# Optimization experiments

Hardware: AMD Instinct MI355X
Metric: run time of the kernel (lower is better)

The kernel has to match this reference:

```python
import jax, jax.numpy as jnp
import numpy as np

WS = 7          # window size (fixed: last_idx=169=(2*7-1)^2)
NP = 1          # num_priorset
NH = 8          # num heads
DIM = 256
SHIFT = 3
N = WS * WS     # 49 tokens per window
NK = N + 3 * NP # 52 K/V tokens (window + uk/fg/bg priors)


def _rel_index():
    coords = np.stack(np.meshgrid(np.arange(WS), np.arange(WS), indexing='ij')).reshape(2, -1)
    rel = (coords[:, :, None] - coords[:, None, :]).transpose(1, 2, 0).astype(np.int64)
    rel[:, :, 0] += WS - 1
    rel[:, :, 1] += WS - 1
    rel[:, :, 0] *= 2 * WS - 1
    idx = rel.sum(-1)                      # (49,49) in [0,168]
    full = np.full((N, NK), 169, dtype=np.int64)
    full[:, :N] = idx
    for j in range(3 * NP):
        full[:, N + j] = 169 + j           # dedicated bias rows for priors
    return jnp.asarray(full)

REL_IDX = _rel_index()


def _ln(t, g, b, eps=1e-5):
    mu = t.mean(-1, keepdims=True)
    var = ((t - mu) ** 2).mean(-1, keepdims=True)
    return (t - mu) * jax.lax.rsqrt(var + eps) * g + b


def setup_inputs() -> dict:
    key = jax.random.key(0)
    ks = jax.random.split(key, 16)
    B, H, W, C = 4, 112, 112, DIM
    nW = (H // WS) * (W // WS)
    hid = 4 * C
    inp = {
        'x': jax.random.normal(ks[0], (B, H * W, C), jnp.float32),
        'mask_matrix': jax.random.normal(ks[1], (nW, N, N), jnp.float32),
        'area_fg': jax.random.uniform(ks[2], (B, H, W, 1), jnp.float32),
        'area_bg': jax.random.uniform(ks[3], (B, H, W, 1), jnp.float32),
        'area_uk': jax.random.uniform(ks[4], (B, H, W, 1), jnp.float32),
        'norm1_g': jnp.ones((C,), jnp.float32),
        'norm1_b': jnp.zeros((C,), jnp.float32),
        'norm2_g': jnp.ones((C,), jnp.float32),
        'norm2_b': jnp.zeros((C,), jnp.float32),
        'qkv_w': jax.random.normal(ks[5], (3 * C, C), jnp.float32) * 0.02,
        'qkv_b': jnp.zeros((3 * C,), jnp.float32),
        'proj_w': jax.random.normal(ks[6], (C, C), jnp.float32) * 0.02,
        'proj_b': jnp.zeros((C,), jnp.float32),
        'rel_table': jax.random.normal(ks[7], (169 + 3 * NP, NH), jnp.float32) * 0.02,
        'fc1_w': jax.random.normal(ks[8], (hid, C), jnp.float32) * 0.02,
        'fc1_b': jnp.zeros((hid,), jnp.float32),
        'fc2_w': jax.random.normal(ks[9], (C, hid), jnp.float32) * 0.02,
        'fc2_b': jnp.zeros((C,), jnp.float32),
        'H': 112,
        'W': 112,
    }
    return inp


def reference(x, mask_matrix, area_fg, area_bg, area_uk,
              norm1_g, norm1_b, norm2_g, norm2_b,
              qkv_w, qkv_b, proj_w, proj_b, rel_table,
              fc1_w, fc1_b, fc2_w, fc2_b, H, W):
    B, L, C = x.shape
    d = C // NH
    scale = d ** -0.5
    nWh, nWw = H // WS, W // WS
    nW = nWh * nWw

    shortcut = x
    x4 = x.reshape(B, H, W, C)
    eps = 1e-9
    # masked global-average prior tokens (B, C)
    def pooled(area):
        return (area * x4).sum((1, 2)) / (area.sum((1, 2)) + eps)
    uk, fg, bg = pooled(area_uk), pooled(area_fg), pooled(area_bg)

    xn = _ln(x, norm1_g, norm1_b).reshape(B, H, W, C)
    uk_n = _ln(uk, norm1_g, norm1_b)
    fg_n = _ln(fg, norm1_g, norm1_b)
    bg_n = _ln(bg, norm1_g, norm1_b)

    # cyclic shift + window partition (H,W divisible by WS -> no padding)
    xs = jnp.roll(xn, (-SHIFT, -SHIFT), (1, 2))
    xw = xs.reshape(B, nWh, WS, nWw, WS, C).transpose(0, 1, 3, 2, 4, 5).reshape(B * nW, N, C)

    # prior highway tokens (order: unknown, fg, bg) and per-window copies
    ph = jnp.stack([uk_n, fg_n, bg_n], axis=1)                      # (B,3,C)
    pr = jnp.broadcast_to(ph[:, None], (B, nW, 3, C)).reshape(B * nW, 3, C)
    xk = jnp.concatenate([xw, pr], axis=1)                          # (B_,52,C)

    qkv = (xk @ qkv_w.T + qkv_b).reshape(B * nW, NK, 3, NH, d)
    q = qkv[:, :N, 0].transpose(0, 2, 1, 3) * scale                 # (B_,h,49,d)
    k = qkv[:, :, 1].transpose(0, 2, 1, 3)                          # (B_,h,52,d)
    v = qkv[:, :, 2].transpose(0, 2, 1, 3)

    attn = jnp.einsum('bhnd,bhmd->bhnm', q, k)                      # (B_,h,49,52)
    bias = rel_table[REL_IDX].transpose(2, 0, 1)                    # (h,49,52)
    attn = attn + bias[None]
    mask = jnp.pad(mask_matrix, ((0, 0), (0, 0), (0, 3 * NP)))      # (nW,49,52)
    attn = attn.reshape(B, nW, NH, N, NK) + mask[None, :, None]
    attn = jax.nn.softmax(attn.reshape(B * nW, NH, N, NK), axis=-1)

    out = jnp.einsum('bhnm,bhmd->bhnd', attn, v)
    out = out.transpose(0, 2, 1, 3).reshape(B * nW, N, C)
    out = out @ proj_w.T + proj_b

    # prior highway: qkv on priors, keep V, project
    ph_qkv = (ph @ qkv_w.T + qkv_b).reshape(B, 3 * NP, 3, NH, d)
    v_hw = ph_qkv[:, :, 2].reshape(B, 3 * NP, C) @ proj_w.T + proj_b

    # window reverse + reverse shift
    xo = out.reshape(B, nWh, nWw, WS, WS, C).transpose(0, 1, 3, 2, 4, 5).reshape(B, H, W, C)
    xo = jnp.roll(xo, (SHIFT, SHIFT), (1, 2)).reshape(B, L, C)

    x = shortcut + xo
    h = _ln(x, norm2_g, norm2_b)
    h = jax.nn.gelu(h @ fc1_w.T + fc1_b, approximate=False)
    x = x + (h @ fc2_w.T + fc2_b)
    return x, v_hw
```

## Files before the change

kernel.cpp:

```cpp
#include <hip/hip_runtime.h>
#include <hip/hip_bf16.h>
#include <math.h>

typedef __bf16 bf16;
typedef bf16 bf16x8 __attribute__((ext_vector_type(8)));
typedef bf16 bf16x4 __attribute__((ext_vector_type(4)));
typedef float f32x4 __attribute__((ext_vector_type(4)));

constexpr int DIM   = 256;
constexpr int NH    = 8;
constexpr int LTOT  = 112 * 112;
constexpr int BTOT  = 4;
constexpr int MROWS = BTOT * LTOT;
constexpr int MQKV  = MROWS + BTOT * 3;
constexpr int NTOK  = 49;
constexpr int NKV   = 52;

__global__ __launch_bounds__(256) void cvt_all(
    const float* __restrict__ qkvw, const float* __restrict__ projw,
    const float* __restrict__ fc1w, const float* __restrict__ fc2w,
    bf16* __restrict__ d)
{
    int i = blockIdx.x * 256 + threadIdx.x;
    float v;
    if (i < 196608)      v = qkvw[i];
    else if (i < 262144) v = projw[i - 196608];
    else if (i < 524288) v = fc1w[i - 262144];
    else                 v = fc2w[i - 524288];
    d[i] = (bf16)v;
}

__global__ __launch_bounds__(256) void pool_partial(
    const float* __restrict__ x, const float* __restrict__ afg,
    const float* __restrict__ abg, const float* __restrict__ auk,
    float* __restrict__ pnum, float* __restrict__ pden)
{
    int b = blockIdx.x / 196, ch = blockIdx.x % 196;
    int p0 = ch * 64, tid = threadIdx.x;
    __shared__ float su[64], sf[64], sb[64];
    if (tid < 64) {
        int p = p0 + tid;
        su[tid] = auk[b * LTOT + p];
        sf[tid] = afg[b * LTOT + p];
        sb[tid] = abg[b * LTOT + p];
    }
    __syncthreads();
    float nu = 0.f, nf = 0.f, nb = 0.f;
    const float* xp = x + ((size_t)b * LTOT + p0) * DIM + tid;
    for (int pp = 0; pp < 64; ++pp) {
        float xv = xp[(size_t)pp * DIM];
        nu += su[pp] * xv; nf += sf[pp] * xv; nb += sb[pp] * xv;
    }
    size_t base = (size_t)blockIdx.x * 3 * DIM + tid;
    pnum[base]           = nu;
    pnum[base + DIM]     = nf;
    pnum[base + 2 * DIM] = nb;
    if (tid < 3) {
        const float* sptr = tid == 0 ? su : (tid == 1 ? sf : sb);
        float t = 0.f;
        for (int i = 0; i < 64; ++i) t += sptr[i];
        pden[blockIdx.x * 3 + tid] = t;
    }
}

__device__ __forceinline__ void block_meanvar(float v, float& mu, float& rstd, float eps) {
    float s = v, s2 = v * v;
    #pragma unroll
    for (int o = 32; o >= 1; o >>= 1) { s += __shfl_down(s, o); s2 += __shfl_down(s2, o); }
    __shared__ float ps[4], ps2[4];
    int w = threadIdx.x >> 6, ln = threadIdx.x & 63;
    if (ln == 0) { ps[w] = s; ps2[w] = s2; }
    __syncthreads();
    float S  = ps[0] + ps[1] + ps[2] + ps[3];
    float S2 = ps2[0] + ps2[1] + ps2[2] + ps2[3];
    mu = S * (1.f / 256.f);
    float var = S2 * (1.f / 256.f) - mu * mu;
    rstd = rsqrtf(var + eps);
}

__global__ __launch_bounds__(256) void prior_ln(
    const float* __restrict__ pnum, const float* __restrict__ pden,
    const float* __restrict__ g, const float* __restrict__ bt, bf16* __restrict__ xn)
{
    int b = blockIdx.x / 3, j = blockIdx.x % 3, tid = threadIdx.x;
    float s = 0.f, den = 0.f;
    for (int ch = 0; ch < 196; ++ch) {
        s   += pnum[((size_t)(b * 196 + ch) * 3 + j) * DIM + tid];
        den += pden[(b * 196 + ch) * 3 + j];
    }
    float v = s / (den + 1e-9f);
    float mu, rs;
    block_meanvar(v, mu, rs, 1e-5f);
    xn[((size_t)MROWS + blockIdx.x) * DIM + tid] = (bf16)((v - mu) * rs * g[tid] + bt[tid]);
}

__global__ __launch_bounds__(512) void ln1_kernel(
    const float* __restrict__ x, const float* __restrict__ g,
    const float* __restrict__ bt, bf16* __restrict__ xn)
{
    const size_t row = (size_t)blockIdx.x * 8 + (threadIdx.x >> 6);
    const int lane = threadIdx.x & 63;
    f32x4 v = *(const f32x4*)(x + row * DIM + lane * 4);
    float s  = v[0] + v[1] + v[2] + v[3];
    float s2 = v[0]*v[0] + v[1]*v[1] + v[2]*v[2] + v[3]*v[3];
    #pragma unroll
    for (int o = 32; o >= 1; o >>= 1) { s += __shfl_xor(s, o); s2 += __shfl_xor(s2, o); }
    float mu = s * (1.f / 256.f);
    float var = s2 * (1.f / 256.f) - mu * mu;
    float rs = rsqrtf(var + 1e-5f);
    f32x4 gv = *(const f32x4*)(g + lane * 4);
    f32x4 bv = *(const f32x4*)(bt + lane * 4);
    bf16x4 o;
    #pragma unroll
    for (int u = 0; u < 4; ++u) o[u] = (bf16)((v[u] - mu) * rs * gv[u] + bv[u]);
    *(bf16x4*)(xn + row * DIM + lane * 4) = o;
}

__device__ __forceinline__ void load_lds16(const void* g, void* l) {
    __builtin_amdgcn_global_load_lds((const __attribute__((address_space(1))) void*)g,
                                     (__attribute__((address_space(3))) void*)l, 16, 0, 0);
}

template <int EPI, int K, int N>
__global__ __launch_bounds__(256) void gemm_bt(
    const bf16* __restrict__ A, const bf16* __restrict__ W,
    const float* __restrict__ bias, bf16* __restrict__ Cb,
    float* __restrict__ Cf, const float* __restrict__ resid, int M)
{
    __shared__ __align__(16) char smem[49152];
    const int tid = threadIdx.x;
    const int wv = tid >> 6, lane = tid & 63;

    const int gx = gridDim.x;
    const int nwg = gx * (int)gridDim.y;
    int lin = blockIdx.y * gx + blockIdx.x;
    int xcd = lin & 7, loc = lin >> 3;
    int qq = nwg >> 3, rr = nwg & 7;
    int nid = (xcd < rr ? xcd * (qq + 1) : rr * (qq + 1) + (xcd - rr) * qq) + loc;
    int by = nid / gx, bx = nid - by * gx;
    const int m0 = by * 128, n0 = bx * 128;

    const int r  = tid >> 2;
    const int kb = (((tid & 3) ^ ((tid >> 3) & 3)) * 8);
    const int wr = (wv >> 1) * 64, wc = (wv & 1) * 64;
    const int fr = lane & 15;
    const int fo = (((lane >> 4) ^ ((fr >> 1) & 3)) * 8);

    int ra0 = m0 + r;      if (ra0 >= M) ra0 = M - 1;
    int ra1 = m0 + r + 64; if (ra1 >= M) ra1 = M - 1;
    const bf16* pA0 = A + (size_t)ra0 * K + kb;
    const bf16* pA1 = A + (size_t)ra1 * K + kb;
    const bf16* pW0 = W + (size_t)(n0 + r) * K + kb;
    const bf16* pW1 = W + (size_t)(n0 + r + 64) * K + kb;

    const f32x4 zero = {0.f, 0.f, 0.f, 0.f};
    f32x4 acc[4][4];
    #pragma unroll
    for (int i = 0; i < 4; ++i)
        #pragma unroll
        for (int j = 0; j < 4; ++j) acc[i][j] = zero;

    constexpr int nK = K >> 5;

    auto stage = [&](int kt, int b) {
        bf16* Ab = (bf16*)(smem + b * 16384);
        bf16* Bb = (bf16*)(smem + b * 16384 + 8192);
        const int off = kt * 32;
        load_lds16(pA0 + off, Ab + wv * 512);
        load_lds16(pA1 + off, Ab + 2048 + wv * 512);
        load_lds16(pW0 + off, Bb + wv * 512);
        load_lds16(pW1 + off, Bb + 2048 + wv * 512);
    };

    stage(0, 0);
    stage(1, 1);

    #pragma unroll
    for (int kt = 0; kt < nK; ++kt) {
        const int cur = kt % 3;
        asm volatile("s_waitcnt lgkmcnt(0)" ::: "memory");
        if (kt < nK - 1) asm volatile("s_waitcnt vmcnt(4)" ::: "memory");
        else             asm volatile("s_waitcnt vmcnt(0)" ::: "memory");
        __builtin_amdgcn_s_barrier();
        if (kt + 2 < nK) stage(kt + 2, (kt + 2) % 3);
        const bf16* Ac = (const bf16*)(smem + cur * 16384);
        const bf16* Bc = (const bf16*)(smem + cur * 16384 + 8192);
        bf16x8 af[4], bw[4];
        #pragma unroll
        for (int i = 0; i < 4; ++i) af[i] = *(const bf16x8*)(Ac + (wr + i * 16 + fr) * 32 + fo);
        #pragma unroll
        for (int i = 0; i < 4; ++i) bw[i] = *(const bf16x8*)(Bc + (wc + i * 16 + fr) * 32 + fo);
        #pragma unroll
        for (int i = 0; i < 4; ++i)
            #pragma unroll
            for (int j = 0; j < 4; ++j)
                acc[i][j] = __builtin_amdgcn_mfma_f32_16x16x32_bf16(af[i], bw[j], acc[i][j], 0, 0, 0);
    }
    __syncthreads();

    const int cr = (lane >> 4) * 4, cc = lane & 15;
    if constexpr (EPI == 3) {
        float* Cs = (float*)smem;
        #pragma unroll
        for (int half = 0; half < 2; ++half) {
            if (wr == half * 64) {
                #pragma unroll
                for (int i = 0; i < 4; ++i)
                    #pragma unroll
                    for (int j = 0; j < 4; ++j) {
                        const int col = wc + j * 16 + cc;
                        const float bv = bias[n0 + col];
                        #pragma unroll
                        for (int q = 0; q < 4; ++q)
                            Cs[(i * 16 + cr + q) * 132 + col] = acc[i][j][q] + bv;
                    }
            }
            __syncthreads();
            for (int p = tid; p < 2048; p += 256) {
                const int row = p >> 5, seg = (p & 31) * 4;
                const int gr = m0 + half * 64 + row;
                if (gr < M) {
                    f32x4 v = *(const f32x4*)(Cs + row * 132 + seg);
                    const size_t o = (size_t)gr * N + n0 + seg;
                    f32x4 rv = *(const f32x4*)(resid + o);
                    *(f32x4*)(Cf + o) = v + rv;
                }
            }
            __syncthreads();
        }
    } else {
        bf16* Csb = (bf16*)smem;
        #pragma unroll
        for (int i = 0; i < 4; ++i)
            #pragma unroll
            for (int j = 0; j < 4; ++j) {
                const int col = wc + j * 16 + cc;
                const float bv = bias[n0 + col];
                #pragma unroll
                for (int q = 0; q < 4; ++q) {
                    float v = acc[i][j][q] + bv;
                    if constexpr (EPI == 2) {
                        float u = 0.7978845608028654f * (v + 0.044715f * v * v * v);
                        v = v / (1.f + __expf(-2.f * u));
                    }
                    Csb[(wr + i * 16 + cr + q) * 144 + col] = (bf16)v;
                }
            }
        __syncthreads();
        for (int p = tid; p < 2048; p += 256) {
            const int row = p >> 4, seg = (p & 15) * 8;
            const int gr = m0 + row;
            if (gr < M)
                *(bf16x8*)(Cb + (size_t)gr * N + n0 + seg) = *(const bf16x8*)(Csb + row * 144 + seg);
        }
    }
}

__global__ __launch_bounds__(256) void proj_ln2(
    const bf16* __restrict__ A, const bf16* __restrict__ W,
    const float* __restrict__ bias, const float* __restrict__ x,
    const float* __restrict__ g, const float* __restrict__ bt,
    float* __restrict__ x2, bf16* __restrict__ ln2)
{
    __shared__ __align__(16) char smem[40960];
    bf16* As = (bf16*)smem;
    bf16* Bs = (bf16*)(smem + 8192);

    const int tid = threadIdx.x;
    const int wv = tid >> 6, lane = tid & 63;
    const int m0 = blockIdx.x * 64;

    const int r4 = tid >> 2;
    const int kb = (((tid & 3) ^ ((tid >> 3) & 3)) * 8);
    const int fr = lane & 15;
    const int fo = (((lane >> 4) ^ ((fr >> 1) & 3)) * 8);

    const bf16* pA  = A + (size_t)(m0 + r4) * 256 + kb;
    const bf16* pW0 = W + (size_t)(r4)       * 256 + kb;
    const bf16* pW1 = W + (size_t)(r4 + 64)  * 256 + kb;
    const bf16* pW2 = W + (size_t)(r4 + 128) * 256 + kb;
    const bf16* pW3 = W + (size_t)(r4 + 192) * 256 + kb;

    const f32x4 zero = {0.f, 0.f, 0.f, 0.f};
    f32x4 acc[4][4];
    #pragma unroll
    for (int i = 0; i < 4; ++i)
        #pragma unroll
        for (int j = 0; j < 4; ++j) acc[i][j] = zero;

    auto stage = [&](int kt, int b) {
        const int off = kt * 32;
        load_lds16(pA  + off, As + b * 2048 + wv * 512);
        load_lds16(pW0 + off, Bs + b * 8192 + wv * 512);
        load_lds16(pW1 + off, Bs + b * 8192 + 2048 + wv * 512);
        load_lds16(pW2 + off, Bs + b * 8192 + 4096 + wv * 512);
        load_lds16(pW3 + off, Bs + b * 8192 + 6144 + wv * 512);
    };

    stage(0, 0);
    __syncthreads();
    #pragma unroll
    for (int kt = 0; kt < 8; ++kt) {
        const int cur = kt & 1;
        if (kt + 1 < 8) stage(kt + 1, cur ^ 1);
        const bf16* Ac = As + cur * 2048;
        const bf16* Bc = Bs + cur * 8192;
        bf16x8 af[4], bw[4];
        #pragma unroll
        for (int i = 0; i < 4; ++i) af[i] = *(const bf16x8*)(Ac + (i * 16 + fr) * 32 + fo);
        #pragma unroll
        for (int j = 0; j < 4; ++j) bw[j] = *(const bf16x8*)(Bc + (wv * 64 + j * 16 + fr) * 32 + fo);
        #pragma unroll
        for (int i = 0; i < 4; ++i)
            #pragma unroll
            for (int j = 0; j < 4; ++j)
                acc[i][j] = __builtin_amdgcn_mfma_f32_16x16x32_bf16(af[i], bw[j], acc[i][j], 0, 0, 0);
        __syncthreads();
    }

    float* Cs = (float*)smem;
    const int cr = (lane >> 4) * 4, cc = lane & 15;
    const f32x4 gv  = *(const f32x4*)(g  + lane * 4);
    const f32x4 bv2 = *(const f32x4*)(bt + lane * 4);
    #pragma unroll
    for (int h = 0; h < 2; ++h) {
        #pragma unroll
        for (int i2 = 0; i2 < 2; ++i2) {
            const int i = h * 2 + i2;
            #pragma unroll
            for (int j = 0; j < 4; ++j) {
                const int col = wv * 64 + j * 16 + cc;
                const float bv = bias[col];
                #pragma unroll
                for (int q = 0; q < 4; ++q)
                    Cs[(i2 * 16 + cr + q) * 260 + col] = acc[i][j][q] + bv;
            }
        }
        __syncthreads();
        #pragma unroll
        for (int it = 0; it < 8; ++it) {
            const int rl = wv * 8 + it;
            const int ar = m0 + h * 32 + rl;
            int bwin = ar / 49;
            int n = ar - bwin * 49;
            int bb = bwin >> 8, w = bwin & 255;
            int ni = n / 7, nj = n - ni * 7;
            int hh = (w >> 4) * 7 + ni + 3;  if (hh >= 112) hh -= 112;
            int ww2 = (w & 15) * 7 + nj + 3; if (ww2 >= 112) ww2 -= 112;
            const size_t nrow = (size_t)(bb * LTOT + hh * 112 + ww2);
            f32x4 pv = *(const f32x4*)(Cs + rl * 260 + lane * 4);
            f32x4 xv = *(const f32x4*)(x + nrow * 256 + lane * 4);
            f32x4 v = pv + xv;
            float s1 = v[0] + v[1] + v[2] + v[3];
            float s2 = v[0]*v[0] + v[1]*v[1] + v[2]*v[2] + v[3]*v[3];
            #pragma unroll
            for (int o = 32; o >= 1; o >>= 1) { s1 += __shfl_xor(s1, o); s2 += __shfl_xor(s2, o); }
            float mu = s1 * (1.f / 256.f);
            float rs = rsqrtf(s2 * (1.f / 256.f) - mu * mu + 1e-5f);
            *(f32x4*)(x2 + nrow * 256 + lane * 4) = v;
            bf16x4 ov;
            #pragma unroll
            for (int u = 0; u < 4; ++u) ov[u] = (bf16)((v[u] - mu) * rs * gv[u] + bv2[u]);
            *(bf16x4*)(ln2 + nrow * 256 + lane * 4) = ov;
        }
        __syncthreads();
    }
}

__device__ __forceinline__ unsigned pk2(float a, float b) {
    union { bf16 h[2]; unsigned u; } c;
    c.h[0] = (bf16)a; c.h[1] = (bf16)b;
    return c.u;
}

__global__ __launch_bounds__(512, 2) void attn_kernel(
    const bf16* __restrict__ qkv, const float* __restrict__ mask,
    const float* __restrict__ rel, bf16* __restrict__ att_out)
{
    __shared__ int rowtab[52];
    __shared__ float mLds[64 * 67];
    __shared__ float rLds[1376];
    __shared__ __align__(16) bf16 vT[8 * 32 * 80];

    const int tid = threadIdx.x;
    const int bw = blockIdx.x;
    const int b = bw >> 8, w = bw & 255;
    const int wh = w >> 4, wwi = w & 15;

    if (tid < 52) {
        int row;
        if (tid < 49) {
            int i = tid / 7, j = tid % 7;
            int gh = wh * 7 + i + 3;  if (gh >= 112) gh -= 112;
            int gw = wwi * 7 + j + 3; if (gw >= 112) gw -= 112;
            row = b * LTOT + gh * 112 + gw;
        } else {
            row = MROWS + b * 3 + (tid - 49);
        }
        rowtab[tid] = row;
    }
    __syncthreads();

    for (int e = tid; e < 64 * 67; e += 512) {
        int q = e / 67, k = e % 67;
        mLds[e] = (q < 49 && k < 49) ? mask[(size_t)w * 2401 + q * 49 + k] : 0.f;
    }
    for (int e = tid; e < 1376; e += 512) rLds[e] = rel[e];
    for (int e = tid; e < 256 * 12; e += 512) {
        int rr = e / 12, c = 52 + e % 12;
        vT[rr * 80 + c] = (bf16)0.f;
    }
    for (int e = tid; e < 52 * 256; e += 512) {
        int key = e >> 8, c = e & 255;
        vT[c * 80 + key] = qkv[(size_t)rowtab[key] * 768 + 512 + c];
    }
    __syncthreads();

    const int h    = tid >> 6;
    const int lane = tid & 63;
    const int cl   = lane & 15;
    const int hi4  = lane >> 4;
    const int cr   = hi4 * 4;
    const int fo   = hi4 * 8;

    bf16x8 kf[4], qf[4];
    #pragma unroll
    for (int i = 0; i < 4; ++i) {
        int key = 16 * i + cl; if (key > 51) key = 51;
        kf[i] = *(const bf16x8*)(qkv + (size_t)rowtab[key] * 768 + 256 + h * 32 + fo);
    }
    #pragma unroll
    for (int j = 0; j < 4; ++j) {
        int qq = 16 * j + cl; if (qq > 48) qq = 48;
        qf[j] = *(const bf16x8*)(qkv + (size_t)rowtab[qq] * 768 + h * 32 + fo);
    }
    const f32x4 zero = {0.f, 0.f, 0.f, 0.f};
    f32x4 acc[4][4];
    #pragma unroll
    for (int i = 0; i < 4; ++i)
        #pragma unroll
        for (int j = 0; j < 4; ++j) acc[i][j] = zero;
    __builtin_amdgcn_s_setprio(1);
    #pragma unroll
    for (int i = 0; i < 4; ++i)
        #pragma unroll
        for (int j = 0; j < 4; ++j)
            acc[i][j] = __builtin_amdgcn_mfma_f32_16x16x32_bf16(kf[i], qf[j], acc[i][j], 0, 0, 0);
    __builtin_amdgcn_s_setprio(0);

    int kb[4][4];
    #pragma unroll
    for (int i = 0; i < 4; ++i)
        #pragma unroll
        for (int r = 0; r < 4; ++r) {
            int key = 16 * i + cr + r;
            kb[i][r] = (key / 7) * 13 + (key % 7);
        }

    f32x4 oacc[4][2];
    #pragma unroll
    for (int i = 0; i < 4; ++i) { oacc[i][0] = zero; oacc[i][1] = zero; }

    #pragma unroll
    for (int j = 0; j < 4; ++j) {
        const int q = 16 * j + cl;
        const int i1 = q / 7, j1 = q % 7;
        const int qb = (i1 + 6) * 13 + (j1 + 6);
        float sv[16];
        float mx = -3e38f;
        #pragma unroll
        for (int i = 0; i < 4; ++i)
            #pragma unroll
            for (int r = 0; r < 4; ++r) {
                int key = 16 * i + cr + r;
                int idx = key < 49 ? (qb - kb[i][r]) : (169 + key - 49);
                idx = idx < 0 ? 0 : (idx > 171 ? 171 : idx);
                float s = acc[i][j][r] * 0.17677669529663687f
                        + mLds[q * 67 + key] + rLds[idx * 8 + h];
                if (key >= 52) s = -3e38f;
                sv[i * 4 + r] = s;
                mx = fmaxf(mx, s);
            }
        mx = fmaxf(mx, __shfl_xor(mx, 16));
        mx = fmaxf(mx, __shfl_xor(mx, 32));
        float sum = 0.f;
        #pragma unroll
        for (int e = 0; e < 16; ++e) { float p = __expf(sv[e] - mx); sv[e] = p; sum += p; }
        sum += __shfl_xor(sum, 16);
        sum += __shfl_xor(sum, 32);
        const float inv = 1.f / sum;

        int Dw[4][2];
        #pragma unroll
        for (int i = 0; i < 4; ++i) {
            Dw[i][0] = pk2(sv[i * 4 + 0] * inv, sv[i * 4 + 1] * inv);
            Dw[i][1] = pk2(sv[i * 4 + 2] * inv, sv[i * 4 + 3] * inv);
        }
        #pragma unroll
        for (int ks = 0; ks < 2; ++ks) {
            int paw[4];
            #pragma unroll
            for (int m = 0; m < 4; ++m) {
                const int srcLane = cl + (((hi4 & 1) * 2 + (m >> 1)) << 4);
                int va = __shfl(Dw[2 * ks][m & 1], srcLane);
                int vb = __shfl(Dw[2 * ks + 1][m & 1], srcLane);
                paw[m] = (hi4 & 2) ? vb : va;
            }
            union { int w[4]; bf16x8 v; } pf;
            pf.w[0] = paw[0]; pf.w[1] = paw[1]; pf.w[2] = paw[2]; pf.w[3] = paw[3];
            bf16x8 vf0 = *(const bf16x8*)(vT + (h * 32 + cl)      * 80 + 32 * ks + fo);
            bf16x8 vf1 = *(const bf16x8*)(vT + (h * 32 + 16 + cl) * 80 + 32 * ks + fo);
            __builtin_amdgcn_s_setprio(1);
            oacc[j][0] = __builtin_amdgcn_mfma_f32_16x16x32_bf16(pf.v, vf0, oacc[j][0], 0, 0, 0);
            oacc[j][1] = __builtin_amdgcn_mfma_f32_16x16x32_bf16(pf.v, vf1, oacc[j][1], 0, 0, 0);
            __builtin_amdgcn_s_setprio(0);
        }
    }

    #pragma unroll
    for (int i = 0; i < 4; ++i)
        #pragma unroll
        for (int r = 0; r < 4; ++r) {
            int q = 16 * i + cr + r;
            if (q < 49) {
                bf16* op = att_out + ((size_t)bw * 49 + q) * 256 + h * 32 + cl;
                op[0]  = (bf16)oacc[i][0][r];
                op[16] = (bf16)oacc[i][1][r];
            }
        }
}

__global__ __launch_bounds__(256) void vhw_kernel(
    const bf16* __restrict__ qkv, const float* __restrict__ pw,
    const float* __restrict__ pb, float* __restrict__ outp)
{
    int rowI = blockIdx.x;
    int c = threadIdx.x;
    const bf16* vp = qkv + (size_t)(MROWS + rowI) * 768 + 512;
    const float* wr_ = pw + (size_t)c * DIM;
    float acc = pb[c];
    for (int k = 0; k < DIM; ++k) acc += (float)vp[k] * wr_[k];
    outp[(size_t)rowI * DIM + c] = acc;
}

extern "C" void kernel_launch(void* const* d_in, const int* in_sizes, int n_in,
                              void* d_out, int out_size, void* d_ws, size_t ws_size,
                              hipStream_t stream)
{
    const float* x     = (const float*)d_in[0];
    const float* mask  = (const float*)d_in[1];
    const float* afg   = (const float*)d_in[2];
    const float* abg   = (const float*)d_in[3];
    const float* auk   = (const float*)d_in[4];
    const float* n1g   = (const float*)d_in[5];
    const float* n1b   = (const float*)d_in[6];
    const float* n2g   = (const float*)d_in[7];
    const float* n2b   = (const float*)d_in[8];
    const float* qkvw  = (const float*)d_in[9];
    const float* qkvb  = (const float*)d_in[10];
    const float* projw = (const float*)d_in[11];
    const float* projb = (const float*)d_in[12];
    const float* rel   = (const float*)d_in[13];
    const float* fc1w  = (const float*)d_in[14];
    const float* fc1b  = (const float*)d_in[15];
    const float* fc2w  = (const float*)d_in[16];
    const float* fc2b  = (const float*)d_in[17];
    float* out = (float*)d_out;
    char*  ws  = (char*)d_ws;

    bf16*  wq   = (bf16*)(ws + 0);
    bf16*  wp   = (bf16*)(ws + 393216);
    bf16*  wf1  = (bf16*)(ws + 524288);
    bf16*  wf2  = (bf16*)(ws + 1048576);
    float* pnum = (float*)(ws + (28ull << 20));
    float* pden = (float*)(ws + (28ull << 20) + 2408448);
    bf16* xn    = (bf16*)(ws + (2ull << 20));
    bf16* atto  = (bf16*)(ws + (2ull << 20));
    bf16* hbuf  = (bf16*)(ws + (2ull << 20));
    bf16* qkvo  = (bf16*)(ws + (28ull << 20));
    bf16* ln2b  = (bf16*)(ws + (102ull << 20));

    cvt_all<<<3072, 256, 0, stream>>>(qkvw, projw, fc1w, fc2w, (bf16*)ws);

    pool_partial<<<BTOT * 196, 256, 0, stream>>>(x, afg, abg, auk, pnum, pden);
    prior_ln<<<12, 256, 0, stream>>>(pnum, pden, n1g, n1b, xn);
    ln1_kernel<<<MROWS / 8, 512, 0, stream>>>(x, n1g, n1b, xn);

    gemm_bt<0, 256, 768><<<dim3(6, 393), 256, 0, stream>>>(xn, wq, qkvb, qkvo, nullptr, nullptr, MQKV);

    attn_kernel<<<BTOT * 256, 512, 0, stream>>>(qkvo, mask, rel, atto);
    vhw_kernel<<<12, 256, 0, stream>>>(qkvo, projw, projb, out + (size_t)MROWS * DIM);

    proj_ln2<<<MROWS / 64, 256, 0, stream>>>(atto, wp, projb, x, n2g, n2b, out, ln2b);

    gemm_bt<2, 256, 1024><<<dim3(8, 392), 256, 0, stream>>>(ln2b, wf1, fc1b, hbuf, nullptr, nullptr, MROWS);

    gemm_bt<3, 1024, 256><<<dim3(2, 392), 256, 0, stream>>>(hbuf, wf2, fc2b, nullptr, out, out, MROWS);

    (void)in_sizes; (void)n_in; (void)out_size; (void)ws_size;
}
```

Before: 282.0 us.

## Merge prologue kernels, fold vhw into attention, and shrink attention LDS footprint

Combines weight conversion, pooling partials and LN1 into one launch dispatched by block index, and folds the prior-highway V projection into extra blocks of the attention kernel. This removes three kernel launches and lets the small independent jobs run alongside the larger ones. Attention LDS is trimmed (mask 49x53, V transpose stride 72) and launch bounds are raised so more blocks fit per CU. The tighter stride may cause LDS bank conflicts, and the higher occupancy target may cause register spills.

```diff
diff --git a/kernel.cpp b/kernel.cpp
--- a/kernel.cpp
+++ b/kernel.cpp
@@ -16,51 +16,76 @@
 constexpr int NTOK  = 49;
 constexpr int NKV   = 52;
 
-__global__ __launch_bounds__(256) void cvt_all(
+__global__ __launch_bounds__(512) void prologue(
     const float* __restrict__ qkvw, const float* __restrict__ projw,
     const float* __restrict__ fc1w, const float* __restrict__ fc2w,
-    bf16* __restrict__ d)
-{
-    int i = blockIdx.x * 256 + threadIdx.x;
-    float v;
-    if (i < 196608)      v = qkvw[i];
-    else if (i < 262144) v = projw[i - 196608];
-    else if (i < 524288) v = fc1w[i - 262144];
-    else                 v = fc2w[i - 524288];
-    d[i] = (bf16)v;
-}
-
-__global__ __launch_bounds__(256) void pool_partial(
+    bf16* __restrict__ wdst,
     const float* __restrict__ x, const float* __restrict__ afg,
     const float* __restrict__ abg, const float* __restrict__ auk,
-    float* __restrict__ pnum, float* __restrict__ pden)
+    float* __restrict__ pnum, float* __restrict__ pden,
+    const float* __restrict__ g, const float* __restrict__ bt,
+    bf16* __restrict__ xn)
 {
-    int b = blockIdx.x / 196, ch = blockIdx.x % 196;
-    int p0 = ch * 64, tid = threadIdx.x;
-    __shared__ float su[64], sf[64], sb[64];
-    if (tid < 64) {
-        int p = p0 + tid;
-        su[tid] = auk[b * LTOT + p];
-        sf[tid] = afg[b * LTOT + p];
-        sb[tid] = abg[b * LTOT + p];
-    }
-    __syncthreads();
-    float nu = 0.f, nf = 0.f, nb = 0.f;
-    const float* xp = x + ((size_t)b * LTOT + p0) * DIM + tid;
-    for (int pp = 0; pp < 64; ++pp) {
-        float xv = xp[(size_t)pp * DIM];
-        nu += su[pp] * xv; nf += sf[pp] * xv; nb += sb[pp] * xv;
-    }
-    size_t base = (size_t)blockIdx.x * 3 * DIM + tid;
-    pnum[base]           = nu;
-    pnum[base + DIM]     = nf;
-    pnum[base + 2 * DIM] = nb;
-    if (tid < 3) {
-        const float* sptr = tid == 0 ? su : (tid == 1 ? sf : sb);
-        float t = 0.f;
-        for (int i = 0; i < 64; ++i) t += sptr[i];
-        pden[blockIdx.x * 3 + tid] = t;
-    }
+    const int blk = blockIdx.x;
+    const int tid = threadIdx.x;
+    if (blk < 1536) {
+        int i = blk * 512 + tid;
+        float v;
+        if (i < 196608)      v = qkvw[i];
+        else if (i < 262144) v = projw[i - 196608];
+        else if (i < 524288) v = fc1w[i - 262144];
+        else                 v = fc2w[i - 524288];
+        wdst[i] = (bf16)v;
+        return;
+    }
+    if (blk < 2320) {
+        const int pb = blk - 1536;
+        const int b = pb / 196, ch = pb % 196;
+        const int p0 = ch * 64;
+        __shared__ float su[64], sf[64], sb[64];
+        if (tid < 64) {
+            int p = p0 + tid;
+            su[tid] = auk[b * LTOT + p];
+            sf[tid] = afg[b * LTOT + p];
+            sb[tid] = abg[b * LTOT + p];
+        }
+        __syncthreads();
+        if (tid < 256) {
+            float nu = 0.f, nf = 0.f, nb = 0.f;
+            const float* xp = x + ((size_t)b * LTOT + p0) * DIM + tid;
+            for (int pp = 0; pp < 64; ++pp) {
+                float xv = xp[(size_t)pp * DIM];
+                nu += su[pp] * xv; nf += sf[pp] * xv; nb += sb[pp] * xv;
+            }
+            size_t base = (size_t)pb * 3 * DIM + tid;
+            pnum[base]           = nu;
+            pnum[base + DIM]     = nf;
+            pnum[base + 2 * DIM] = nb;
+            if (tid < 3) {
+                const float* sptr = tid == 0 ? su : (tid == 1 ? sf : sb);
+                float t = 0.f;
+                for (int i = 0; i < 64; ++i) t += sptr[i];
+                pden[pb * 3 + tid] = t;
+            }
+        }
+        return;
+    }
+    const size_t row = (size_t)(blk - 2320) * 8 + (tid >> 6);
+    const int lane = tid & 63;
+    f32x4 v = *(const f32x4*)(x + row * DIM + lane * 4);
+    float s  = v[0] + v[1] + v[2] + v[3];
+    float s2 = v[0]*v[0] + v[1]*v[1] + v[2]*v[2] + v[3]*v[3];
+    #pragma unroll
+    for (int o = 32; o >= 1; o >>= 1) { s += __shfl_xor(s, o); s2 += __shfl_xor(s2, o); }
+    float mu = s * (1.f / 256.f);
+    float var = s2 * (1.f / 256.f) - mu * mu;
+    float rs = rsqrtf(var + 1e-5f);
+    f32x4 gv = *(const f32x4*)(g + lane * 4);
+    f32x4 bv = *(const f32x4*)(bt + lane * 4);
+    bf16x4 o;
+    #pragma unroll
+    for (int u = 0; u < 4; ++u) o[u] = (bf16)((v[u] - mu) * rs * gv[u] + bv[u]);
+    *(bf16x4*)(xn + row * DIM + lane * 4) = o;
 }
 
 __device__ __forceinline__ void block_meanvar(float v, float& mu, float& rstd, float eps) {
@@ -92,28 +117,6 @@
     float mu, rs;
     block_meanvar(v, mu, rs, 1e-5f);
     xn[((size_t)MROWS + blockIdx.x) * DIM + tid] = (bf16)((v - mu) * rs * g[tid] + bt[tid]);
-}
-
-__global__ __launch_bounds__(512) void ln1_kernel(
-    const float* __restrict__ x, const float* __restrict__ g,
-    const float* __restrict__ bt, bf16* __restrict__ xn)
-{
-    const size_t row = (size_t)blockIdx.x * 8 + (threadIdx.x >> 6);
-    const int lane = threadIdx.x & 63;
-    f32x4 v = *(const f32x4*)(x + row * DIM + lane * 4);
-    float s  = v[0] + v[1] + v[2] + v[3];
-    float s2 = v[0]*v[0] + v[1]*v[1] + v[2]*v[2] + v[3]*v[3];
-    #pragma unroll
-    for (int o = 32; o >= 1; o >>= 1) { s += __shfl_xor(s, o); s2 += __shfl_xor(s2, o); }
-    float mu = s * (1.f / 256.f);
-    float var = s2 * (1.f / 256.f) - mu * mu;
-    float rs = rsqrtf(var + 1e-5f);
-    f32x4 gv = *(const f32x4*)(g + lane * 4);
-    f32x4 bv = *(const f32x4*)(bt + lane * 4);
-    bf16x4 o;
-    #pragma unroll
-    for (int u = 0; u < 4; ++u) o[u] = (bf16)((v[u] - mu) * rs * gv[u] + bv[u]);
-    *(bf16x4*)(xn + row * DIM + lane * 4) = o;
 }
 
 __device__ __forceinline__ void load_lds16(const void* g, void* l) {
@@ -373,17 +376,32 @@
     return c.u;
 }
 
-__global__ __launch_bounds__(512, 2) void attn_kernel(
+__global__ __launch_bounds__(512, 6) void attn_kernel(
     const bf16* __restrict__ qkv, const float* __restrict__ mask,
-    const float* __restrict__ rel, bf16* __restrict__ att_out)
+    const float* __restrict__ rel, bf16* __restrict__ att_out,
+    const float* __restrict__ pw, const float* __restrict__ pb,
+    float* __restrict__ vhw_out)
 {
-    __shared__ int rowtab[52];
-    __shared__ float mLds[64 * 67];
-    __shared__ float rLds[1376];
-    __shared__ __align__(16) bf16 vT[8 * 32 * 80];
-
     const int tid = threadIdx.x;
     const int bw = blockIdx.x;
+
+    if (bw >= 1024) {
+        if (tid < 256) {
+            const int rowI = bw - 1024;
+            const bf16* vp = qkv + (size_t)(MROWS + rowI) * 768 + 512;
+            const float* wr_ = pw + (size_t)tid * DIM;
+            float acc = pb[tid];
+            for (int k = 0; k < DIM; ++k) acc += (float)vp[k] * wr_[k];
+            vhw_out[(size_t)rowI * DIM + tid] = acc;
+        }
+        return;
+    }
+
+    __shared__ int rowtab[52];
+    __shared__ float mLds[49 * 53];
+    __shared__ float rLds[1376];
+    __shared__ __align__(16) bf16 vT[256 * 72];
+
     const int b = bw >> 8, w = bw & 255;
     const int wh = w >> 4, wwi = w & 15;
 
@@ -401,18 +419,18 @@
     }
     __syncthreads();
 
-    for (int e = tid; e < 64 * 67; e += 512) {
-        int q = e / 67, k = e % 67;
-        mLds[e] = (q < 49 && k < 49) ? mask[(size_t)w * 2401 + q * 49 + k] : 0.f;
+    for (int e = tid; e < 49 * 53; e += 512) {
+        int q = e / 53, k = e % 53;
+        mLds[e] = (k < 49) ? mask[(size_t)w * 2401 + q * 49 + k] : 0.f;
     }
     for (int e = tid; e < 1376; e += 512) rLds[e] = rel[e];
     for (int e = tid; e < 256 * 12; e += 512) {
         int rr = e / 12, c = 52 + e % 12;
-        vT[rr * 80 + c] = (bf16)0.f;
+        vT[rr * 72 + c] = (bf16)0.f;
     }
     for (int e = tid; e < 52 * 256; e += 512) {
         int key = e >> 8, c = e & 255;
-        vT[c * 80 + key] = qkv[(size_t)rowtab[key] * 768 + 512 + c];
+        vT[c * 72 + key] = qkv[(size_t)rowtab[key] * 768 + 512 + c];
     }
     __syncthreads();
 
@@ -464,6 +482,7 @@
     #pragma unroll
     for (int j = 0; j < 4; ++j) {
         const int q = 16 * j + cl;
+        const int qc = q > 48 ? 48 : q;
         const int i1 = q / 7, j1 = q % 7;
         const int qb = (i1 + 6) * 13 + (j1 + 6);
         float sv[16];
@@ -476,7 +495,7 @@
                 int idx = key < 49 ? (qb - kb[i][r]) : (169 + key - 49);
                 idx = idx < 0 ? 0 : (idx > 171 ? 171 : idx);
                 float s = acc[i][j][r] * 0.17677669529663687f
-                        + mLds[q * 67 + key] + rLds[idx * 8 + h];
+                        + mLds[qc * 53 + key] + rLds[idx * 8 + h];
                 if (key >= 52) s = -3e38f;
                 sv[i * 4 + r] = s;
                 mx = fmaxf(mx, s);
@@ -508,8 +527,8 @@
             }
             union { int w[4]; bf16x8 v; } pf;
             pf.w[0] = paw[0]; pf.w[1] = paw[1]; pf.w[2] = paw[2]; pf.w[3] = paw[3];
-            bf16x8 vf0 = *(const bf16x8*)(vT + (h * 32 + cl)      * 80 + 32 * ks + fo);
-            bf16x8 vf1 = *(const bf16x8*)(vT + (h * 32 + 16 + cl) * 80 + 32 * ks + fo);
+            bf16x8 vf0 = *(const bf16x8*)(vT + (h * 32 + cl)      * 72 + 32 * ks + fo);
+            bf16x8 vf1 = *(const bf16x8*)(vT + (h * 32 + 16 + cl) * 72 + 32 * ks + fo);
             __builtin_amdgcn_s_setprio(1);
             oacc[j][0] = __builtin_amdgcn_mfma_f32_16x16x32_bf16(pf.v, vf0, oacc[j][0], 0, 0, 0);
             oacc[j][1] = __builtin_amdgcn_mfma_f32_16x16x32_bf16(pf.v, vf1, oacc[j][1], 0, 0, 0);
@@ -528,19 +547,6 @@
                 op[16] = (bf16)oacc[i][1][r];
             }
         }
-}
-
-__global__ __launch_bounds__(256) void vhw_kernel(
-    const bf16* __restrict__ qkv, const float* __restrict__ pw,
-    const float* __restrict__ pb, float* __restrict__ outp)
-{
-    int rowI = blockIdx.x;
-    int c = threadIdx.x;
-    const bf16* vp = qkv + (size_t)(MROWS + rowI) * 768 + 512;
-    const float* wr_ = pw + (size_t)c * DIM;
-    float acc = pb[c];
-    for (int k = 0; k < DIM; ++k) acc += (float)vp[k] * wr_[k];
-    outp[(size_t)rowI * DIM + c] = acc;
 }
 
 extern "C" void kernel_launch(void* const* d_in, const int* in_sizes, int n_in,
@@ -580,16 +586,14 @@
     bf16* qkvo  = (bf16*)(ws + (28ull << 20));
     bf16* ln2b  = (bf16*)(ws + (102ull << 20));
 
-    cvt_all<<<3072, 256, 0, stream>>>(qkvw, projw, fc1w, fc2w, (bf16*)ws);
-
-    pool_partial<<<BTOT * 196, 256, 0, stream>>>(x, afg, abg, auk, pnum, pden);
+    prologue<<<8592, 512, 0, stream>>>(qkvw, projw, fc1w, fc2w, (bf16*)ws,
+                                       x, afg, abg, auk, pnum, pden, n1g, n1b, xn);
     prior_ln<<<12, 256, 0, stream>>>(pnum, pden, n1g, n1b, xn);
-    ln1_kernel<<<MROWS / 8, 512, 0, stream>>>(x, n1g, n1b, xn);
 
     gemm_bt<0, 256, 768><<<dim3(6, 393), 256, 0, stream>>>(xn, wq, qkvb, qkvo, nullptr, nullptr, MQKV);
 
-    attn_kernel<<<BTOT * 256, 512, 0, stream>>>(qkvo, mask, rel, atto);
-    vhw_kernel<<<12, 256, 0, stream>>>(qkvo, projw, projb, out + (size_t)MROWS * DIM);
+    attn_kernel<<<1024 + 12, 512, 0, stream>>>(qkvo, mask, rel, atto,
+                                               projw, projb, out + (size_t)MROWS * DIM);
 
     proj_ln2<<<MROWS / 64, 256, 0, stream>>>(atto, wp, projb, x, n2g, n2b, out, ln2b);
 
```

Measured after the change: 332.0 us. 1.18x slower.
